# Performance work log

Measured on AMD Instinct MI355X. Metric: run time of the kernel, lower is better.

The kernel has to match this reference:

```python
import jax, jax.numpy as jnp
import numpy as np

N_ATOMS = 100000
N_EDGES = 400000
ATOM_DIM = 32
BOND_DIM = 16


def setup_inputs() -> dict:
    key = jax.random.key(0)
    k1, k2, k3, k4 = jax.random.split(key, 4)
    atom_features = jax.random.normal(k1, (N_ATOMS, ATOM_DIM), dtype=jnp.float32)
    bond_features = jax.random.normal(k2, (N_EDGES, BOND_DIM), dtype=jnp.float32)
    pair_indices = jax.random.randint(k3, (N_EDGES, 2), 0, N_ATOMS, dtype=jnp.int64)
    # glorot-uniform-like scale for the kernel
    limit = np.sqrt(6.0 / (BOND_DIM + ATOM_DIM * ATOM_DIM)).astype(np.float32)
    kernel = jax.random.uniform(k4, (BOND_DIM, ATOM_DIM * ATOM_DIM), dtype=jnp.float32,
                                minval=-limit, maxval=limit)
    bias = jnp.zeros((ATOM_DIM * ATOM_DIM,), dtype=jnp.float32)
    return {"atom_features": atom_features, "bond_features": bond_features,
            "pair_indices": pair_indices, "kernel": kernel, "bias": bias}


def reference(atom_features, bond_features, pair_indices, kernel, bias):
    n_atoms, d = atom_features.shape  # d = atom_dim
    e = bond_features.shape[0]
    # per-edge transform matrices: [E, d, d]
    edge_mats = (bond_features @ kernel + bias).reshape(e, d, d)
    # gather neighbor atom features via pair_indices[:, 1]
    neighbors = atom_features[pair_indices[:, 1]]  # [E, d]
    # per-edge matvec
    transformed = jnp.einsum('eij,ej->ei', edge_mats, neighbors)  # [E, d]
    # scatter-reduce onto source atoms
    return jax.ops.segment_sum(transformed, pair_indices[:, 0], num_segments=n_atoms)
```

## Files before the change

kernel.cpp:

```cpp
#include <hip/hip_runtime.h>


typedef _Float16 half8 __attribute__((ext_vector_type(8)));
typedef _Float16 half4t __attribute__((ext_vector_type(4)));
typedef float float4v __attribute__((ext_vector_type(4)));

constexpr int NA = 100000;
constexpr int E  = 400000;
constexpr int TILES = E / 32;
constexpr int NBLK  = 1536;
constexpr int HALFW = NBLK * 4 / 2;

constexpr size_t OFF_ATOMH = 0;
constexpr size_t OFF_BONDH = (size_t)NA * 32 * 2;

constexpr int NZ4 = NA * 32 / 4;
constexpr int NA4 = NA * 32 / 4;
constexpr int NB4 = E * 16 / 4;
constexpr int PREP_TOT = NZ4 + NA4 + NB4;

__global__ void k_prep(const float* __restrict__ atom,
                       const float* __restrict__ bond,
                       float4* __restrict__ outz,
                       half4t* __restrict__ atomh4,
                       half4t* __restrict__ bondh4) {
  int i = blockIdx.x * blockDim.x + threadIdx.x;
  if (i < NZ4) {
    outz[i] = make_float4(0.f, 0.f, 0.f, 0.f);
  } else if (i < NZ4 + NA4) {
    int k = i - NZ4;
    float4 v = ((const float4*)atom)[k];
    half4t hh = { (_Float16)v.x, (_Float16)v.y, (_Float16)v.z, (_Float16)v.w };
    atomh4[k] = hh;
  } else if (i < PREP_TOT) {
    int k = i - NZ4 - NA4;
    float4 v = ((const float4*)bond)[k];
    half4t hh = { (_Float16)v.x, (_Float16)v.y, (_Float16)v.z, (_Float16)v.w };
    bondh4[k] = hh;
  }
}

static __device__ inline half8 splat8(_Float16 v) {
  half8 r = {v, v, v, v, v, v, v, v};
  return r;
}

__global__ __launch_bounds__(256, 3)
void edge_fused(const _Float16* __restrict__ atomh,
                const _Float16* __restrict__ bondh,
                const int* __restrict__ pairs,
                const float* __restrict__ Kmat,
                const float* __restrict__ bias,
                float* __restrict__ out)
{
  const int tid  = threadIdx.x;
  const int lane = tid & 63;
  const int wid  = blockIdx.x * 4 + (tid >> 6);
  const int h    = wid & 1;
  const int q    = lane >> 4;
  const int el   = lane & 15;
  const int n    = el + h * 16;
  const int j0   = q * 8;

  half8 Wr[17];
  #pragma unroll
  for (int s = 0; s < 17; ++s) {
    const float* src = (s < 16) ? (Kmat + s * 1024 + n * 32 + j0)
                                : (bias + n * 32 + j0);
    half8 w;
    #pragma unroll
    for (int j = 0; j < 8; ++j) w[j] = (_Float16)src[j];
    Wr[s] = w;
  }

  const int start  = wid >> 1;
  const int stride = HALFW;
  const int2* pairs2 = (const int2*)pairs;

  auto ldpv = [&](int t) -> int2 {
    const int tc = t < TILES ? t : TILES - 1;
    int2 v = make_int2(0, 0);
    if (lane < 32) v = pairs2[tc * 32 + lane];
    return v;
  };

  if (start >= TILES) return;

  int2 pv0 = ldpv(start);
  int2 pv1 = ldpv(start + stride);

  half8 nbA_c, nbB_c, bA0_c, bA1_c, bB0_c, bB1_c;
  {
    const int aA = __shfl(pv0.y, el);
    const int aB = __shfl(pv0.y, el + 16);
    nbA_c = *(const half8*)(atomh + (size_t)aA * 32 + j0);
    nbB_c = *(const half8*)(atomh + (size_t)aB * 32 + j0);
    const _Float16* brA = bondh + (size_t)(start * 32 + el) * 16;
    const _Float16* brB = bondh + (size_t)(start * 32 + el + 16) * 16;
    bA0_c = *(const half8*)(brA);  bA1_c = *(const half8*)(brA + 8);
    bB0_c = *(const half8*)(brB);  bB1_c = *(const half8*)(brB + 8);
  }

  for (int t = start; t < TILES; t += stride) {
    const int tn = t + stride;

    half8 nbA_n, nbB_n, bA0_n, bA1_n, bB0_n, bB1_n;
    {
      const int aA = __shfl(pv1.y, el);
      const int aB = __shfl(pv1.y, el + 16);
      nbA_n = *(const half8*)(atomh + (size_t)aA * 32 + j0);
      nbB_n = *(const half8*)(atomh + (size_t)aB * 32 + j0);
      const int tc = tn < TILES ? tn : TILES - 1;
      const _Float16* brA = bondh + (size_t)(tc * 32 + el) * 16;
      const _Float16* brB = bondh + (size_t)(tc * 32 + el + 16) * 16;
      bA0_n = *(const half8*)(brA);  bA1_n = *(const half8*)(brA + 8);
      bB0_n = *(const half8*)(brB);  bB1_n = *(const half8*)(brB + 8);
    }
    const int2 pv2 = ldpv(tn + stride);

    float4v acc0 = {0.f, 0.f, 0.f, 0.f};
    float4v acc1 = {0.f, 0.f, 0.f, 0.f};
    #pragma unroll
    for (int s = 0; s < 16; ++s) {
      const _Float16 sA = (s < 8) ? bA0_c[s] : bA1_c[s - 8];
      const _Float16 sB = (s < 8) ? bB0_c[s] : bB1_c[s - 8];
      const half8 aAf = nbA_c * splat8(sA);
      const half8 aBf = nbB_c * splat8(sB);
      acc0 = __builtin_amdgcn_mfma_f32_16x16x32_f16(aAf, Wr[s], acc0, 0, 0, 0);
      acc1 = __builtin_amdgcn_mfma_f32_16x16x32_f16(aBf, Wr[s], acc1, 0, 0, 0);
    }
    acc0 = __builtin_amdgcn_mfma_f32_16x16x32_f16(nbA_c, Wr[16], acc0, 0, 0, 0);
    acc1 = __builtin_amdgcn_mfma_f32_16x16x32_f16(nbB_c, Wr[16], acc1, 0, 0, 0);

    #pragma unroll
    for (int r = 0; r < 4; ++r) {
      const int s0 = __shfl(pv0.x, q * 4 + r);
      atomicAdd(out + (size_t)s0 * 32 + n, acc0[r]);
      const int s1 = __shfl(pv0.x, q * 4 + r + 16);
      atomicAdd(out + (size_t)s1 * 32 + n, acc1[r]);
    }

    pv0 = pv1; pv1 = pv2;
    nbA_c = nbA_n; nbB_c = nbB_n;
    bA0_c = bA0_n; bA1_c = bA1_n; bB0_c = bB0_n; bB1_c = bB1_n;
  }
}

extern "C" void kernel_launch(void* const* d_in, const int* in_sizes, int n_in,
                              void* d_out, int out_size, void* d_ws, size_t ws_size,
                              hipStream_t stream) {
  const float* atom  = (const float*)d_in[0];
  const float* bondf = (const float*)d_in[1];
  const int*   pairs = (const int*)d_in[2];
  const float* Kmat  = (const float*)d_in[3];
  const float* bias  = (const float*)d_in[4];
  float* out = (float*)d_out;

  _Float16* atomh = (_Float16*)((char*)d_ws + OFF_ATOMH);
  _Float16* bondh = (_Float16*)((char*)d_ws + OFF_BONDH);

  k_prep<<<(PREP_TOT + 255) / 256, 256, 0, stream>>>(
      atom, bondf, (float4*)out, (half4t*)atomh, (half4t*)bondh);
  edge_fused<<<NBLK, 256, 0, stream>>>(atomh, bondh, pairs, Kmat, bias, out);
}
```

Measured before the change: 143.3 us.

## Scatter into fp16 accumulator with packed half2 atomics, convert at end

Replaces per-element fp32 atomicAdds on the output with packed half2 atomic adds into a workspace fp16 accumulator. Lanes exchange values via shuffles so each lane issues one atomic covering two adjacent columns, which halves the atomic count and the scatter footprint. A final kernel converts the fp16 accumulator back to fp32 output. This risks precision loss from accumulating segment sums in fp16 and adds an extra launch plus a conversion pass.

```diff
diff --git a/kernel.cpp b/kernel.cpp
--- a/kernel.cpp
+++ b/kernel.cpp
@@ -1,8 +1,10 @@
 #include <hip/hip_runtime.h>
+#include <hip/hip_fp16.h>
 
 
 typedef _Float16 half8 __attribute__((ext_vector_type(8)));
 typedef _Float16 half4t __attribute__((ext_vector_type(4)));
+typedef _Float16 half2t __attribute__((ext_vector_type(2)));
 typedef float float4v __attribute__((ext_vector_type(4)));
 
 constexpr int NA = 100000;
@@ -13,30 +15,38 @@
 
 constexpr size_t OFF_ATOMH = 0;
 constexpr size_t OFF_BONDH = (size_t)NA * 32 * 2;
+constexpr size_t OFF_ACCH  = OFF_BONDH + (size_t)E * 16 * 2;
 
-constexpr int NZ4 = NA * 32 / 4;
-constexpr int NA4 = NA * 32 / 4;
-constexpr int NB4 = E * 16 / 4;
-constexpr int PREP_TOT = NZ4 + NA4 + NB4;
+constexpr int NACC4 = NA * 32 / 8;
+constexpr int NA4   = NA * 32 / 4;
+constexpr int NB4   = E * 16 / 4;
+constexpr int PREP_TOT = NACC4 + NA4 + NB4;
 
 __global__ void k_prep(const float* __restrict__ atom,
                        const float* __restrict__ bond,
-                       float4* __restrict__ outz,
+                       float4* __restrict__ acchz,
                        half4t* __restrict__ atomh4,
                        half4t* __restrict__ bondh4) {
   int i = blockIdx.x * blockDim.x + threadIdx.x;
-  if (i < NZ4) {
-    outz[i] = make_float4(0.f, 0.f, 0.f, 0.f);
-  } else if (i < NZ4 + NA4) {
-    int k = i - NZ4;
+  if (i < NACC4) {
+    acchz[i] = make_float4(0.f, 0.f, 0.f, 0.f);
+  } else if (i < NACC4 + NA4) {
+    int k = i - NACC4;
     float4 v = ((const float4*)atom)[k];
     half4t hh = { (_Float16)v.x, (_Float16)v.y, (_Float16)v.z, (_Float16)v.w };
     atomh4[k] = hh;
   } else if (i < PREP_TOT) {
-    int k = i - NZ4 - NA4;
+    int k = i - NACC4 - NA4;
     float4 v = ((const float4*)bond)[k];
     half4t hh = { (_Float16)v.x, (_Float16)v.y, (_Float16)v.z, (_Float16)v.w };
     bondh4[k] = hh;
+  }
+}
+
+__global__ void k_final(const __half2* __restrict__ acch2, float2* __restrict__ out2) {
+  int i = blockIdx.x * blockDim.x + threadIdx.x;
+  if (i < NA * 16) {
+    out2[i] = __half22float2(acch2[i]);
   }
 }
 
@@ -51,7 +61,7 @@
                 const int* __restrict__ pairs,
                 const float* __restrict__ Kmat,
                 const float* __restrict__ bias,
-                float* __restrict__ out)
+                _Float16* __restrict__ acch)
 {
   const int tid  = threadIdx.x;
   const int lane = tid & 63;
@@ -101,6 +111,8 @@
     bB0_c = *(const half8*)(brB);  bB1_c = *(const half8*)(brB + 8);
   }
 
+  const bool evenLane = (lane & 1) == 0;
+
   for (int t = start; t < TILES; t += stride) {
     const int tn = t + stride;
 
@@ -134,10 +146,17 @@
 
     #pragma unroll
     for (int r = 0; r < 4; ++r) {
+      const float pA = __shfl_xor(acc0[r], 1);
+      const float pB = __shfl_xor(acc1[r], 1);
       const int s0 = __shfl(pv0.x, q * 4 + r);
-      atomicAdd(out + (size_t)s0 * 32 + n, acc0[r]);
       const int s1 = __shfl(pv0.x, q * 4 + r + 16);
-      atomicAdd(out + (size_t)s1 * 32 + n, acc1[r]);
+      const int sdst = evenLane ? s0 : s1;
+      const int col  = evenLane ? n : (n - 1);
+      const float lo = evenLane ? acc0[r] : pB;
+      const float hi = evenLane ? pA : acc1[r];
+      half2t hv = { (_Float16)lo, (_Float16)hi };
+      unsafeAtomicAdd((__half2*)(acch + (size_t)sdst * 32 + col),
+                      __builtin_bit_cast(__half2, hv));
     }
 
     pv0 = pv1; pv1 = pv2;
@@ -158,8 +177,10 @@
 
   _Float16* atomh = (_Float16*)((char*)d_ws + OFF_ATOMH);
   _Float16* bondh = (_Float16*)((char*)d_ws + OFF_BONDH);
+  _Float16* acch  = (_Float16*)((char*)d_ws + OFF_ACCH);
 
   k_prep<<<(PREP_TOT + 255) / 256, 256, 0, stream>>>(
-      atom, bondf, (float4*)out, (half4t*)atomh, (half4t*)bondh);
-  edge_fused<<<NBLK, 256, 0, stream>>>(atomh, bondh, pairs, Kmat, bias, out);
+      atom, bondf, (float4*)acch, (half4t*)atomh, (half4t*)bondh);
+  edge_fused<<<NBLK, 256, 0, stream>>>(atomh, bondh, pairs, Kmat, bias, acch);
+  k_final<<<(NA * 16 + 255) / 256, 256, 0, stream>>>((const __half2*)acch, (float2*)out);
 }
```

Result: slower. 147.3 us (+2.8%).
